# Performance work log

Measured on AMD Instinct MI355X. Metric: run time of the kernel, lower is better.

## Reference

```python
import jax, jax.numpy as jnp
import numpy as np

D = 2048      # in_features (model dim)
H = 1408      # d_intermediate (hidden per expert)
E = 16        # n_routed_experts
T = 16384     # flattened tokens
K = 4         # top_k experts per token


def setup_inputs() -> dict:
    key = jax.random.key(0)
    k1, k2, k3, k4, k5 = jax.random.split(key, 5)
    x = jax.random.normal(k1, (T, D), dtype=jnp.float32)
    weights = jax.random.uniform(k2, (T, K), dtype=jnp.float32)
    indices = jax.random.randint(k3, (T, K), 0, E)
    # Stacked GatedMLP params (bias=False as in mamba's GatedMLP):
    # fc1: [2H, D] per expert, fc2: [D, H] per expert
    W1 = jax.random.normal(k4, (E, 2 * H, D), dtype=jnp.float32) * (D ** -0.5)
    W2 = jax.random.normal(k5, (E, D, H), dtype=jnp.float32) * (H ** -0.5)
    return {"x": x, "weights": weights, "indices": indices, "W1": W1, "W2": W2}


def reference(x, weights, indices, W1, W2):
    # y[t] = sum_i ( GatedMLP_i(x[t]) * sum_k weights[t,k] * [indices[t,k]==i] )
    n_experts = W1.shape[0]
    y = jnp.zeros_like(x)
    for i in range(n_experts):  # small fixed expert loop
        # combined routing weight of expert i per token (handles duplicate hits like += in torch)
        cw = jnp.sum(weights * (indices == i), axis=-1)      # [T]
        h = x @ W1[i].T                                      # [T, 2H]
        u, g = jnp.split(h, 2, axis=-1)                      # chunk(2, dim=-1): (y, gate)
        out = (u * jax.nn.silu(g)) @ W2[i].T                 # [T, D]
        y = y + out * cw[:, None]
    return y
```

## Files before the change

kernel.cpp:

```cpp
#include <hip/hip_runtime.h>

#define D_ 2048
#define H_ 1408
#define E_ 16
#define T_ 16384
#define K_ 4
#define TK_ 65536
#define BM_ 256
#define BK_ 64
#define MAXT_ 272

typedef __attribute__((ext_vector_type(8))) short bf16x8;
typedef __attribute__((ext_vector_type(4))) float f32x4;
typedef __attribute__((ext_vector_type(4))) unsigned short u16x4;
typedef __attribute__((ext_vector_type(8))) unsigned short u16x8;

#define M_COUNTS 0
#define M_OFF    16
#define M_CUR    33
#define M_NT     49
#define M_TE     64
#define M_TR     (64 + MAXT_)
#define M_TN     (64 + 2*MAXT_)

#define XB_OFF   0ULL
#define W1B_OFF  67108864ULL
#define W2B_OFF  (W1B_OFF + 188743680ULL)
#define ACT_OFF  (W2B_OFF + 94371840ULL)
#define PERM_OFF (ACT_OFF + 184549376ULL)
#define WGT_OFF  (PERM_OFF + 262144ULL)
#define META_B   (WGT_OFF + 262144ULL)
#define INV_OFF  (META_B + 65536ULL)
#define YP_OFF   (INV_OFF + 262144ULL)
#define WS_NEED  (YP_OFF + 268435456ULL)

#define SBAR()  __builtin_amdgcn_s_barrier()
#define SCHED() __builtin_amdgcn_sched_barrier(0)
#define LGK0()  asm volatile("s_waitcnt lgkmcnt(0)" ::: "memory")
#define VM6()   asm volatile("s_waitcnt vmcnt(6)" ::: "memory")
#define PRIO1() __builtin_amdgcn_s_setprio(1)
#define PRIO0() __builtin_amdgcn_s_setprio(0)

static __device__ __forceinline__ unsigned short f2bf(float f) {
  unsigned u = __builtin_bit_cast(unsigned, f);
  u += 0x7fffu + ((u >> 16) & 1u);
  return (unsigned short)(u >> 16);
}
static __device__ __forceinline__ float bf2f(unsigned short s) {
  return __builtin_bit_cast(float, (unsigned)s << 16);
}

static __device__ __forceinline__ void gload16(const void* g, unsigned ldsOff) {
  __builtin_amdgcn_global_load_lds(
      (const __attribute__((address_space(1))) unsigned int*)(unsigned long long)g,
      (__attribute__((address_space(3))) unsigned int*)(unsigned long long)ldsOff,
      16, 0, 0);
}

__global__ void cvt_kernel(const float* __restrict__ in,
                           unsigned short* __restrict__ out, long long n) {
  long long i = ((long long)blockIdx.x * blockDim.x + threadIdx.x) * 4;
  const long long stride = (long long)gridDim.x * blockDim.x * 4;
  for (; i < n; i += stride) {
    float4 v = *reinterpret_cast<const float4*>(in + i);
    u16x4 o = { f2bf(v.x), f2bf(v.y), f2bf(v.z), f2bf(v.w) };
    *reinterpret_cast<u16x4*>(out + i) = o;
  }
}

__global__ void route_count(const int* __restrict__ idx, int* __restrict__ meta) {
  int i = blockIdx.x * 256 + threadIdx.x;
  if (i < TK_) atomicAdd(&meta[M_COUNTS + idx[i]], 1);
}

__global__ void scan_build(int* __restrict__ meta) {
  if (threadIdx.x != 0 || blockIdx.x != 0) return;
  int off = 0;
  for (int e = 0; e < E_; ++e) {
    meta[M_OFF + e] = off;
    meta[M_CUR + e] = off;
    off += meta[M_COUNTS + e];
  }
  meta[M_OFF + E_] = off;
  int nt = 0;
  for (int e = 0; e < E_; ++e) {
    int c = meta[M_COUNTS + e], b = meta[M_OFF + e];
    for (int r = 0; r < c; r += BM_) {
      meta[M_TE + nt] = e;
      meta[M_TR + nt] = b + r;
      meta[M_TN + nt] = (c - r < BM_) ? (c - r) : BM_;
      ++nt;
    }
  }
  meta[M_NT] = nt;
}

__global__ void route_fill(const int* __restrict__ idx, const float* __restrict__ wts,
                           int* __restrict__ meta, int* __restrict__ perm,
                           float* __restrict__ wgt, int* __restrict__ inv) {
  int i = blockIdx.x * 256 + threadIdx.x;
  if (i >= TK_) return;
  int e = idx[i];
  int pos = atomicAdd(&meta[M_CUR + e], 1);
  perm[pos] = i >> 2;
  wgt[pos] = wts[i];
  inv[i] = pos;
}

__global__ __launch_bounds__(512, 2) void gemm1_kernel(
    const char* __restrict__ xb, const char* __restrict__ w1b,
    const int* __restrict__ perm, const int* __restrict__ meta,
    unsigned short* __restrict__ act) {
  __shared__ char lds[131072];
  int bid = (int)blockIdx.x;
  bid = (bid & 7) * (int)(gridDim.x >> 3) + (bid >> 3);
  const int tb = bid / 11;
  const int cb = bid - tb * 11;
  if (tb >= meta[M_NT]) return;
  const int e = meta[M_TE + tb];
  const int row0 = meta[M_TR + tb];
  const int nrows = meta[M_TN + tb];
  const int tid = threadIdx.x, lane = tid & 63, wid = tid >> 6;
  const int wr = wid >> 2, wc = wid & 3;
  const unsigned ldsBase = (unsigned)(unsigned long long)&lds[0];
  constexpr int NT = D_ / BK_;

  const char* aSrc[4];
  const char* bSrc[4];
  {
    const int r8 = tid >> 3;
    const unsigned colb0 = (unsigned)(tid & 7) * 16u;
#pragma unroll
    for (int i = 0; i < 4; ++i) {
      const int r = r8 + i * 64;
      const unsigned colb = colb0 ^ ((unsigned)(r & 7) << 4);
      const int rc = (r < nrows) ? r : 0;
      aSrc[i] = xb + (size_t)perm[row0 + rc] * 4096 + colb;
      const int w1row = (i < 2) ? (cb * 128 + r) : (H_ + cb * 128 + (r - 128));
      bSrc[i] = w1b + (size_t)e * (2 * H_) * 4096ULL + (size_t)w1row * 4096 + colb;
    }
  }

  const int l15 = lane & 15, hi = lane >> 4;
  const unsigned swz = (unsigned)(l15 & 7) << 4;
  unsigned aOff[8], bOffU[2], bOffG[2];
#pragma unroll
  for (int m = 0; m < 8; ++m) {
    const int row = wr * 128 + m * 16 + l15;
    aOff[m] = (unsigned)(row * 128) + (((unsigned)hi * 16u) ^ swz);
  }
#pragma unroll
  for (int n = 0; n < 2; ++n) {
    const int ru = wc * 32 + n * 16 + l15;
    bOffU[n] = 65536u + (unsigned)(ru * 128) + (((unsigned)hi * 16u) ^ swz);
    const int rg = ru + 128;
    bOffG[n] = 65536u + (unsigned)(rg * 128) + (((unsigned)hi * 16u) ^ swz);
  }

  f32x4 aU[8][2], aG[8][2];
#pragma unroll
  for (int m = 0; m < 8; ++m)
#pragma unroll
    for (int n = 0; n < 2; ++n) {
      aU[m][n] = (f32x4){0.f, 0.f, 0.f, 0.f};
      aG[m][n] = (f32x4){0.f, 0.f, 0.f, 0.f};
    }

  auto STAGE_A = [&](int t, int h) {
    const int tt = (t < NT) ? t : (NT - 1);
    const size_t kb = (size_t)tt * 128;
    const unsigned dst = ldsBase + (unsigned)(t & 1) * 32768u + (unsigned)h * 16384u + (unsigned)tid * 16u;
    gload16(aSrc[h * 2 + 0] + kb, dst);
    gload16(aSrc[h * 2 + 1] + kb, dst + 8192u);
  };
  auto STAGE_B = [&](int t, int h) {
    const int tt = (t < NT) ? t : (NT - 1);
    const size_t kb = (size_t)tt * 128;
    const unsigned dst = ldsBase + 65536u + (unsigned)(t & 1) * 32768u + (unsigned)h * 16384u + (unsigned)tid * 16u;
    gload16(bSrc[h * 2 + 0] + kb, dst);
    gload16(bSrc[h * 2 + 1] + kb, dst + 8192u);
  };

  STAGE_B(0, 0); STAGE_B(0, 1); STAGE_A(0, 0); STAGE_A(0, 1);
  STAGE_B(1, 0); STAGE_B(1, 1); STAGE_A(1, 0);
  VM6(); SCHED(); SBAR();

  for (int t = 0; t < NT; ++t) {
    const char* base = lds + (unsigned)(t & 1) * 32768u;
    bf16x8 aLo[4][2], aHi[4][2], bu[2][2], bg[2][2];

#pragma unroll
    for (int m = 0; m < 4; ++m)
#pragma unroll
      for (int ks = 0; ks < 2; ++ks)
        aLo[m][ks] = *reinterpret_cast<const bf16x8*>(base + (aOff[m] ^ (unsigned)(ks << 6)));
#pragma unroll
    for (int n = 0; n < 2; ++n)
#pragma unroll
      for (int ks = 0; ks < 2; ++ks)
        bu[n][ks] = *reinterpret_cast<const bf16x8*>(base + (bOffU[n] ^ (unsigned)(ks << 6)));
    STAGE_A(t + 1, 1);
    SCHED(); SBAR(); LGK0(); SCHED();
    PRIO1();
#pragma unroll
    for (int ks = 0; ks < 2; ++ks)
#pragma unroll
      for (int m = 0; m < 4; ++m)
#pragma unroll
        for (int n = 0; n < 2; ++n)
          aU[m][n] = __builtin_amdgcn_mfma_f32_16x16x32_bf16(aLo[m][ks], bu[n][ks], aU[m][n], 0, 0, 0);
    PRIO0(); SCHED(); SBAR();

#pragma unroll
    for (int n = 0; n < 2; ++n)
#pragma unroll
      for (int ks = 0; ks < 2; ++ks)
        bg[n][ks] = *reinterpret_cast<const bf16x8*>(base + (bOffG[n] ^ (unsigned)(ks << 6)));
    STAGE_B(t + 2, 0);
    SCHED(); SBAR(); LGK0(); SCHED();
    PRIO1();
#pragma unroll
    for (int ks = 0; ks < 2; ++ks)
#pragma unroll
      for (int m = 0; m < 4; ++m)
#pragma unroll
        for (int n = 0; n < 2; ++n)
          aG[m][n] = __builtin_amdgcn_mfma_f32_16x16x32_bf16(aLo[m][ks], bg[n][ks], aG[m][n], 0, 0, 0);
    PRIO0(); SCHED(); SBAR();

#pragma unroll
    for (int m = 0; m < 4; ++m)
#pragma unroll
      for (int ks = 0; ks < 2; ++ks)
        aHi[m][ks] = *reinterpret_cast<const bf16x8*>(base + (aOff[4 + m] ^ (unsigned)(ks << 6)));
    STAGE_B(t + 2, 1);
    SCHED(); SBAR(); LGK0(); SCHED();
    PRIO1();
#pragma unroll
    for (int ks = 0; ks < 2; ++ks)
#pragma unroll
      for (int m = 0; m < 4; ++m)
#pragma unroll
        for (int n = 0; n < 2; ++n)
          aU[4 + m][n] = __builtin_amdgcn_mfma_f32_16x16x32_bf16(aHi[m][ks], bu[n][ks], aU[4 + m][n], 0, 0, 0);
    PRIO0(); SCHED(); SBAR();

    STAGE_A(t + 2, 0);
    VM6(); SCHED(); SBAR();
    PRIO1();
#pragma unroll
    for (int ks = 0; ks < 2; ++ks)
#pragma unroll
      for (int m = 0; m < 4; ++m)
#pragma unroll
        for (int n = 0; n < 2; ++n)
          aG[4 + m][n] = __builtin_amdgcn_mfma_f32_16x16x32_bf16(aHi[m][ks], bg[n][ks], aG[4 + m][n], 0, 0, 0);
    PRIO0(); SCHED(); SBAR();
  }

#pragma unroll
  for (int m = 0; m < 8; ++m)
#pragma unroll
    for (int j = 0; j < 4; ++j) {
      const int r = wr * 128 + m * 16 + hi * 4 + j;
      if (r < nrows) {
        const size_t rowBase = (size_t)(row0 + r) * H_ + (size_t)cb * 128 + (size_t)wc * 32;
#pragma unroll
        for (int n = 0; n < 2; ++n) {
          const float u = aU[m][n][j];
          const float g = aG[m][n][j];
          act[rowBase + n * 16 + l15] = f2bf(u * (g / (1.0f + __expf(-g))));
        }
      }
    }
}

template <int ATOMIC>
__global__ __launch_bounds__(512, 2) void gemm2_kernel(
    const char* __restrict__ actb, const char* __restrict__ w2b,
    const int* __restrict__ perm, const float* __restrict__ wgt,
    const int* __restrict__ meta, unsigned short* __restrict__ yp,
    float* __restrict__ y) {
  __shared__ char lds[131072];
  int bid = (int)blockIdx.x;
  bid = (bid & 7) * (int)(gridDim.x >> 3) + (bid >> 3);
  const int tb = bid >> 3;
  const int cb = bid & 7;
  if (tb >= meta[M_NT]) return;
  const int e = meta[M_TE + tb];
  const int row0 = meta[M_TR + tb];
  const int nrows = meta[M_TN + tb];
  const int tid = threadIdx.x, lane = tid & 63, wid = tid >> 6;
  const int wr = wid >> 2, wc = wid & 3;
  const unsigned ldsBase = (unsigned)(unsigned long long)&lds[0];
  constexpr int NT = H_ / BK_;

  const char* aSrc[4];
  const char* bSrc[4];
  {
    const int r8 = tid >> 3;
    const unsigned colb0 = (unsigned)(tid & 7) * 16u;
#pragma unroll
    for (int i = 0; i < 4; ++i) {
      const int r = r8 + i * 64;
      const unsigned colb = colb0 ^ ((unsigned)(r & 7) << 4);
      const int rc = (r < nrows) ? r : 0;
      aSrc[i] = actb + (size_t)(row0 + rc) * (H_ * 2) + colb;
      const int brow = cb * 256 + r;
      bSrc[i] = w2b + (size_t)e * D_ * (H_ * 2) + (size_t)brow * (H_ * 2) + colb;
    }
  }

  const int l15 = lane & 15, hi = lane >> 4;
  const unsigned swz = (unsigned)(l15 & 7) << 4;
  unsigned aOff[8], bOff[4];
#pragma unroll
  for (int m = 0; m < 8; ++m) {
    const int row = wr * 128 + m * 16 + l15;
    aOff[m] = (unsigned)(row * 128) + (((unsigned)hi * 16u) ^ swz);
  }
#pragma unroll
  for (int n = 0; n < 4; ++n) {
    const int rb = wc * 64 + n * 16 + l15;
    bOff[n] = 65536u + (unsigned)(rb * 128) + (((unsigned)hi * 16u) ^ swz);
  }

  f32x4 acc[8][4];
#pragma unroll
  for (int m = 0; m < 8; ++m)
#pragma unroll
    for (int n = 0; n < 4; ++n) acc[m][n] = (f32x4){0.f, 0.f, 0.f, 0.f};

  auto STAGE_A = [&](int t, int h) {
    const int tt = (t < NT) ? t : (NT - 1);
    const size_t kb = (size_t)tt * 128;
    const unsigned dst = ldsBase + (unsigned)(t & 1) * 32768u + (unsigned)h * 16384u + (unsigned)tid * 16u;
    gload16(aSrc[h * 2 + 0] + kb, dst);
    gload16(aSrc[h * 2 + 1] + kb, dst + 8192u);
  };
  auto STAGE_B = [&](int t, int h) {
    const int tt = (t < NT) ? t : (NT - 1);
    const size_t kb = (size_t)tt * 128;
    const unsigned dst = ldsBase + 65536u + (unsigned)(t & 1) * 32768u + (unsigned)h * 16384u + (unsigned)tid * 16u;
    gload16(bSrc[h * 2 + 0] + kb, dst);
    gload16(bSrc[h * 2 + 1] + kb, dst + 8192u);
  };

  STAGE_B(0, 0); STAGE_B(0, 1); STAGE_A(0, 0); STAGE_A(0, 1);
  STAGE_B(1, 0); STAGE_B(1, 1); STAGE_A(1, 0);
  VM6(); SCHED(); SBAR();

  for (int t = 0; t < NT; ++t) {
    const char* base = lds + (unsigned)(t & 1) * 32768u;
    bf16x8 aLo[4][2], aHi[4][2], b[4][2];

#pragma unroll
    for (int m = 0; m < 4; ++m)
#pragma unroll
      for (int ks = 0; ks < 2; ++ks)
        aLo[m][ks] = *reinterpret_cast<const bf16x8*>(base + (aOff[m] ^ (unsigned)(ks << 6)));
#pragma unroll
    for (int n = 0; n < 4; ++n)
#pragma unroll
      for (int ks = 0; ks < 2; ++ks)
        b[n][ks] = *reinterpret_cast<const bf16x8*>(base + (bOff[n] ^ (unsigned)(ks << 6)));
    STAGE_A(t + 1, 1);
    SCHED(); SBAR(); LGK0(); SCHED();
    PRIO1();
#pragma unroll
    for (int ks = 0; ks < 2; ++ks)
#pragma unroll
      for (int m = 0; m < 4; ++m)
#pragma unroll
        for (int n = 0; n < 2; ++n)
          acc[m][n] = __builtin_amdgcn_mfma_f32_16x16x32_bf16(aLo[m][ks], b[n][ks], acc[m][n], 0, 0, 0);
    PRIO0(); SCHED(); SBAR();

    STAGE_B(t + 2, 0);
    SCHED(); SBAR();
    PRIO1();
#pragma unroll
    for (int ks = 0; ks < 2; ++ks)
#pragma unroll
      for (int m = 0; m < 4; ++m)
#pragma unroll
        for (int n = 2; n < 4; ++n)
          acc[m][n] = __builtin_amdgcn_mfma_f32_16x16x32_bf16(aLo[m][ks], b[n][ks], acc[m][n], 0, 0, 0);
    PRIO0(); SCHED(); SBAR();

#pragma unroll
    for (int m = 0; m < 4; ++m)
#pragma unroll
      for (int ks = 0; ks < 2; ++ks)
        aHi[m][ks] = *reinterpret_cast<const bf16x8*>(base + (aOff[4 + m] ^ (unsigned)(ks << 6)));
    STAGE_B(t + 2, 1);
    SCHED(); SBAR(); LGK0(); SCHED();
    PRIO1();
#pragma unroll
    for (int ks = 0; ks < 2; ++ks)
#pragma unroll
      for (int m = 0; m < 4; ++m)
#pragma unroll
        for (int n = 0; n < 2; ++n)
          acc[4 + m][n] = __builtin_amdgcn_mfma_f32_16x16x32_bf16(aHi[m][ks], b[n][ks], acc[4 + m][n], 0, 0, 0);
    PRIO0(); SCHED(); SBAR();

    STAGE_A(t + 2, 0);
    VM6(); SCHED(); SBAR();
    PRIO1();
#pragma unroll
    for (int ks = 0; ks < 2; ++ks)
#pragma unroll
      for (int m = 0; m < 4; ++m)
#pragma unroll
        for (int n = 2; n < 4; ++n)
          acc[4 + m][n] = __builtin_amdgcn_mfma_f32_16x16x32_bf16(aHi[m][ks], b[n][ks], acc[4 + m][n], 0, 0, 0);
    PRIO0(); SCHED(); SBAR();
  }

#pragma unroll
  for (int m = 0; m < 8; ++m)
#pragma unroll
    for (int j = 0; j < 4; ++j) {
      const int r = wr * 128 + m * 16 + hi * 4 + j;
      if (r < nrows) {
        const float w = wgt[row0 + r];
        if (ATOMIC) {
          const int token = perm[row0 + r];
          float* yrow = y + (size_t)token * D_ + (size_t)cb * 256 + (size_t)wc * 64;
#pragma unroll
          for (int n = 0; n < 4; ++n)
            unsafeAtomicAdd(&yrow[n * 16 + l15], acc[m][n][j] * w);
        } else {
          unsigned short* prow = yp + (size_t)(row0 + r) * D_ + (size_t)cb * 256 + (size_t)wc * 64;
#pragma unroll
          for (int n = 0; n < 4; ++n)
            prow[n * 16 + l15] = f2bf(acc[m][n][j] * w);
        }
      }
    }
}

__global__ __launch_bounds__(256) void gather_kernel(
    const unsigned short* __restrict__ yp, const int* __restrict__ inv,
    float* __restrict__ y) {
  const int t = blockIdx.x;
  const int d0 = threadIdx.x * 8;
  int pos[4];
#pragma unroll
  for (int k = 0; k < 4; ++k) pos[k] = inv[t * 4 + k];
  float s[8];
#pragma unroll
  for (int i = 0; i < 8; ++i) s[i] = 0.f;
#pragma unroll
  for (int k = 0; k < 4; ++k) {
    u16x8 v = *reinterpret_cast<const u16x8*>(yp + (size_t)pos[k] * D_ + d0);
#pragma unroll
    for (int i = 0; i < 8; ++i) s[i] += bf2f(v[i]);
  }
  float4 lo = {s[0], s[1], s[2], s[3]}, hi4 = {s[4], s[5], s[6], s[7]};
  *reinterpret_cast<float4*>(y + (size_t)t * D_ + d0) = lo;
  *reinterpret_cast<float4*>(y + (size_t)t * D_ + d0 + 4) = hi4;
}

extern "C" void kernel_launch(void* const* d_in, const int* in_sizes, int n_in,
                              void* d_out, int out_size, void* d_ws, size_t ws_size,
                              hipStream_t stream) {
  const float* x   = (const float*)d_in[0];
  const float* wts = (const float*)d_in[1];
  const int*   idx = (const int*)d_in[2];
  const float* W1  = (const float*)d_in[3];
  const float* W2  = (const float*)d_in[4];
  float* y = (float*)d_out;
  char* ws = (char*)d_ws;

  unsigned short* xb  = (unsigned short*)(ws + XB_OFF);
  unsigned short* w1b = (unsigned short*)(ws + W1B_OFF);
  unsigned short* w2b = (unsigned short*)(ws + W2B_OFF);
  unsigned short* act = (unsigned short*)(ws + ACT_OFF);
  int*   perm = (int*)(ws + PERM_OFF);
  float* wgt  = (float*)(ws + WGT_OFF);
  int*   meta = (int*)(ws + META_B);
  int*   inv  = (int*)(ws + INV_OFF);
  unsigned short* yp = (unsigned short*)(ws + YP_OFF);

  const bool useYp = (ws_size >= (size_t)WS_NEED);

  hipMemsetAsync(meta, 0, 64 * sizeof(int), stream);
  if (!useYp) hipMemsetAsync(d_out, 0, (size_t)out_size * sizeof(float), stream);

  cvt_kernel<<<2048, 256, 0, stream>>>(x, xb, (long long)T_ * D_);
  cvt_kernel<<<2048, 256, 0, stream>>>(W1, w1b, (long long)E_ * 2 * H_ * D_);
  cvt_kernel<<<2048, 256, 0, stream>>>(W2, w2b, (long long)E_ * D_ * H_);

  route_count<<<TK_ / 256, 256, 0, stream>>>(idx, meta);
  scan_build<<<1, 64, 0, stream>>>(meta);
  route_fill<<<TK_ / 256, 256, 0, stream>>>(idx, wts, meta, perm, wgt, inv);

  gemm1_kernel<<<MAXT_ * (H_ / 128), 512, 0, stream>>>(
      (const char*)xb, (const char*)w1b, perm, meta, act);

  if (useYp) {
    gemm2_kernel<0><<<MAXT_ * (D_ / 256), 512, 0, stream>>>(
        (const char*)act, (const char*)w2b, perm, wgt, meta, yp, y);
    gather_kernel<<<T_, 256, 0, stream>>>(yp, inv, y);
  } else {
    gemm2_kernel<1><<<MAXT_ * (D_ / 256), 512, 0, stream>>>(
        (const char*)act, (const char*)w2b, perm, wgt, meta, yp, y);
  }
}
```

Baseline: 1.724 ms.

## Fuse fp32-to-bf16 weight conversion into GEMM B-tile loading

Drops the separate cvt passes over W1 and W2. Each GEMM now loads fp32 weight tiles into registers, packs them to bf16 with v_cvt_pk_bf16_f32, and writes them swizzled into LDS, with the wait counts in the pipeline adjusted to match. This removes a full read and write of the weights in bf16 form, but weight tiles are now read in fp32 by every token tile that uses them, which doubles B-side global traffic and adds register and conversion pressure inside the main loop.

```diff
diff --git a/kernel.cpp b/kernel.cpp
--- a/kernel.cpp
+++ b/kernel.cpp
@@ -14,6 +14,7 @@
 typedef __attribute__((ext_vector_type(4))) float f32x4;
 typedef __attribute__((ext_vector_type(4))) unsigned short u16x4;
 typedef __attribute__((ext_vector_type(8))) unsigned short u16x8;
+typedef __attribute__((ext_vector_type(4))) unsigned int u32x4;
 
 #define M_COUNTS 0
 #define M_OFF    16
@@ -24,9 +25,7 @@
 #define M_TN     (64 + 2*MAXT_)
 
 #define XB_OFF   0ULL
-#define W1B_OFF  67108864ULL
-#define W2B_OFF  (W1B_OFF + 188743680ULL)
-#define ACT_OFF  (W2B_OFF + 94371840ULL)
+#define ACT_OFF  67108864ULL
 #define PERM_OFF (ACT_OFF + 184549376ULL)
 #define WGT_OFF  (PERM_OFF + 262144ULL)
 #define META_B   (WGT_OFF + 262144ULL)
@@ -37,7 +36,7 @@
 #define SBAR()  __builtin_amdgcn_s_barrier()
 #define SCHED() __builtin_amdgcn_sched_barrier(0)
 #define LGK0()  asm volatile("s_waitcnt lgkmcnt(0)" ::: "memory")
-#define VM6()   asm volatile("s_waitcnt vmcnt(6)" ::: "memory")
+#define VM10()  asm volatile("s_waitcnt vmcnt(10)" ::: "memory")
 #define PRIO1() __builtin_amdgcn_s_setprio(1)
 #define PRIO0() __builtin_amdgcn_s_setprio(0)
 
@@ -48,6 +47,11 @@
 }
 static __device__ __forceinline__ float bf2f(unsigned short s) {
   return __builtin_bit_cast(float, (unsigned)s << 16);
+}
+static __device__ __forceinline__ unsigned pk2(float lo, float hi) {
+  unsigned r;
+  asm("v_cvt_pk_bf16_f32 %0, %1, %2" : "=v"(r) : "v"(lo), "v"(hi));
+  return r;
 }
 
 static __device__ __forceinline__ void gload16(const void* g, unsigned ldsOff) {
@@ -108,7 +112,7 @@
 }
 
 __global__ __launch_bounds__(512, 2) void gemm1_kernel(
-    const char* __restrict__ xb, const char* __restrict__ w1b,
+    const char* __restrict__ xb, const float* __restrict__ W1,
     const int* __restrict__ perm, const int* __restrict__ meta,
     unsigned short* __restrict__ act) {
   __shared__ char lds[131072];
@@ -126,7 +130,6 @@
   constexpr int NT = D_ / BK_;
 
   const char* aSrc[4];
-  const char* bSrc[4];
   {
     const int r8 = tid >> 3;
     const unsigned colb0 = (unsigned)(tid & 7) * 16u;
@@ -136,9 +139,13 @@
       const unsigned colb = colb0 ^ ((unsigned)(r & 7) << 4);
       const int rc = (r < nrows) ? r : 0;
       aSrc[i] = xb + (size_t)perm[row0 + rc] * 4096 + colb;
-      const int w1row = (i < 2) ? (cb * 128 + r) : (H_ + cb * 128 + (r - 128));
-      bSrc[i] = w1b + (size_t)e * (2 * H_) * 4096ULL + (size_t)w1row * 4096 + colb;
-    }
+    }
+  }
+  const float* bSrcF;
+  {
+    const int r = tid >> 1;
+    const int w1row = (r < 128) ? (cb * 128 + r) : (H_ + cb * 128 + (r - 128));
+    bSrcF = W1 + (size_t)e * (2 * H_) * D_ + (size_t)w1row * D_ + (tid & 1) * 32;
   }
 
   const int l15 = lane & 15, hi = lane >> 4;
@@ -173,17 +180,35 @@
     gload16(aSrc[h * 2 + 0] + kb, dst);
     gload16(aSrc[h * 2 + 1] + kb, dst + 8192u);
   };
-  auto STAGE_B = [&](int t, int h) {
+
+  float4 breg[8];
+  auto B_LOAD = [&](int t) {
     const int tt = (t < NT) ? t : (NT - 1);
-    const size_t kb = (size_t)tt * 128;
-    const unsigned dst = ldsBase + 65536u + (unsigned)(t & 1) * 32768u + (unsigned)h * 16384u + (unsigned)tid * 16u;
-    gload16(bSrc[h * 2 + 0] + kb, dst);
-    gload16(bSrc[h * 2 + 1] + kb, dst + 8192u);
+    const float* p = bSrcF + (size_t)tt * 64;
+#pragma unroll
+    for (int i = 0; i < 8; ++i) breg[i] = *reinterpret_cast<const float4*>(p + i * 4);
   };
-
-  STAGE_B(0, 0); STAGE_B(0, 1); STAGE_A(0, 0); STAGE_A(0, 1);
-  STAGE_B(1, 0); STAGE_B(1, 1); STAGE_A(1, 0);
-  VM6(); SCHED(); SBAR();
+  auto B_WRITE = [&](int t) {
+    char* wb = lds + 65536u + (unsigned)(t & 1) * 32768u + (unsigned)(tid >> 1) * 128u;
+    const unsigned wc0 = (unsigned)(tid & 1) * 64u;
+    const unsigned wsz = ((unsigned)((tid >> 1) & 7)) << 4;
+#pragma unroll
+    for (int j = 0; j < 4; ++j) {
+      u32x4 w;
+      w[0] = pk2(breg[2 * j + 0].x, breg[2 * j + 0].y);
+      w[1] = pk2(breg[2 * j + 0].z, breg[2 * j + 0].w);
+      w[2] = pk2(breg[2 * j + 1].x, breg[2 * j + 1].y);
+      w[3] = pk2(breg[2 * j + 1].z, breg[2 * j + 1].w);
+      *reinterpret_cast<u32x4*>(wb + ((wc0 + (unsigned)j * 16u) ^ wsz)) = w;
+    }
+  };
+
+  B_LOAD(0);
+  STAGE_A(0, 0); STAGE_A(0, 1);
+  B_WRITE(0);
+  B_LOAD(1);
+  STAGE_A(1, 0);
+  VM10(); LGK0(); SCHED(); SBAR();
 
   for (int t = 0; t < NT; ++t) {
     const char* base = lds + (unsigned)(t & 1) * 32768u;
@@ -216,7 +241,7 @@
 #pragma unroll
       for (int ks = 0; ks < 2; ++ks)
         bg[n][ks] = *reinterpret_cast<const bf16x8*>(base + (bOffG[n] ^ (unsigned)(ks << 6)));
-    STAGE_B(t + 2, 0);
+    B_WRITE(t + 1);
     SCHED(); SBAR(); LGK0(); SCHED();
     PRIO1();
 #pragma unroll
@@ -233,7 +258,7 @@
 #pragma unroll
       for (int ks = 0; ks < 2; ++ks)
         aHi[m][ks] = *reinterpret_cast<const bf16x8*>(base + (aOff[4 + m] ^ (unsigned)(ks << 6)));
-    STAGE_B(t + 2, 1);
+    B_LOAD(t + 2);
     SCHED(); SBAR(); LGK0(); SCHED();
     PRIO1();
 #pragma unroll
@@ -246,7 +271,7 @@
     PRIO0(); SCHED(); SBAR();
 
     STAGE_A(t + 2, 0);
-    VM6(); SCHED(); SBAR();
+    VM10(); SCHED(); SBAR();
     PRIO1();
 #pragma unroll
     for (int ks = 0; ks < 2; ++ks)
@@ -277,7 +302,7 @@
 
 template <int ATOMIC>
 __global__ __launch_bounds__(512, 2) void gemm2_kernel(
-    const char* __restrict__ actb, const char* __restrict__ w2b,
+    const char* __restrict__ actb, const float* __restrict__ W2,
     const int* __restrict__ perm, const float* __restrict__ wgt,
     const int* __restrict__ meta, unsigned short* __restrict__ yp,
     float* __restrict__ y) {
@@ -296,7 +321,6 @@
   constexpr int NT = H_ / BK_;
 
   const char* aSrc[4];
-  const char* bSrc[4];
   {
     const int r8 = tid >> 3;
     const unsigned colb0 = (unsigned)(tid & 7) * 16u;
@@ -306,9 +330,13 @@
       const unsigned colb = colb0 ^ ((unsigned)(r & 7) << 4);
       const int rc = (r < nrows) ? r : 0;
       aSrc[i] = actb + (size_t)(row0 + rc) * (H_ * 2) + colb;
-      const int brow = cb * 256 + r;
-      bSrc[i] = w2b + (size_t)e * D_ * (H_ * 2) + (size_t)brow * (H_ * 2) + colb;
-    }
+    }
+  }
+  const float* bSrcF;
+  {
+    const int r = tid >> 1;
+    const int w2row = cb * 256 + r;
+    bSrcF = W2 + (size_t)e * D_ * H_ + (size_t)w2row * H_ + (tid & 1) * 32;
   }
 
   const int l15 = lane & 15, hi = lane >> 4;
@@ -338,17 +366,35 @@
     gload16(aSrc[h * 2 + 0] + kb, dst);
     gload16(aSrc[h * 2 + 1] + kb, dst + 8192u);
   };
-  auto STAGE_B = [&](int t, int h) {
+
+  float4 breg[8];
+  auto B_LOAD = [&](int t) {
     const int tt = (t < NT) ? t : (NT - 1);
-    const size_t kb = (size_t)tt * 128;
-    const unsigned dst = ldsBase + 65536u + (unsigned)(t & 1) * 32768u + (unsigned)h * 16384u + (unsigned)tid * 16u;
-    gload16(bSrc[h * 2 + 0] + kb, dst);
-    gload16(bSrc[h * 2 + 1] + kb, dst + 8192u);
+    const float* p = bSrcF + (size_t)tt * 64;
+#pragma unroll
+    for (int i = 0; i < 8; ++i) breg[i] = *reinterpret_cast<const float4*>(p + i * 4);
   };
-
-  STAGE_B(0, 0); STAGE_B(0, 1); STAGE_A(0, 0); STAGE_A(0, 1);
-  STAGE_B(1, 0); STAGE_B(1, 1); STAGE_A(1, 0);
-  VM6(); SCHED(); SBAR();
+  auto B_WRITE = [&](int t) {
+    char* wb = lds + 65536u + (unsigned)(t & 1) * 32768u + (unsigned)(tid >> 1) * 128u;
+    const unsigned wc0 = (unsigned)(tid & 1) * 64u;
+    const unsigned wsz = ((unsigned)((tid >> 1) & 7)) << 4;
+#pragma unroll
+    for (int j = 0; j < 4; ++j) {
+      u32x4 w;
+      w[0] = pk2(breg[2 * j + 0].x, breg[2 * j + 0].y);
+      w[1] = pk2(breg[2 * j + 0].z, breg[2 * j + 0].w);
+      w[2] = pk2(breg[2 * j + 1].x, breg[2 * j + 1].y);
+      w[3] = pk2(breg[2 * j + 1].z, breg[2 * j + 1].w);
+      *reinterpret_cast<u32x4*>(wb + ((wc0 + (unsigned)j * 16u) ^ wsz)) = w;
+    }
+  };
+
+  B_LOAD(0);
+  STAGE_A(0, 0); STAGE_A(0, 1);
+  B_WRITE(0);
+  B_LOAD(1);
+  STAGE_A(1, 0);
+  VM10(); LGK0(); SCHED(); SBAR();
 
   for (int t = 0; t < NT; ++t) {
     const char* base = lds + (unsigned)(t & 1) * 32768u;
@@ -376,8 +422,8 @@
           acc[m][n] = __builtin_amdgcn_mfma_f32_16x16x32_bf16(aLo[m][ks], b[n][ks], acc[m][n], 0, 0, 0);
     PRIO0(); SCHED(); SBAR();
 
-    STAGE_B(t + 2, 0);
-    SCHED(); SBAR();
+    B_WRITE(t + 1);
+    SCHED(); SBAR(); LGK0(); SCHED();
     PRIO1();
 #pragma unroll
     for (int ks = 0; ks < 2; ++ks)
@@ -393,7 +439,7 @@
 #pragma unroll
       for (int ks = 0; ks < 2; ++ks)
         aHi[m][ks] = *reinterpret_cast<const bf16x8*>(base + (aOff[4 + m] ^ (unsigned)(ks << 6)));
-    STAGE_B(t + 2, 1);
+    B_LOAD(t + 2);
     SCHED(); SBAR(); LGK0(); SCHED();
     PRIO1();
 #pragma unroll
@@ -406,7 +452,7 @@
     PRIO0(); SCHED(); SBAR();
 
     STAGE_A(t + 2, 0);
-    VM6(); SCHED(); SBAR();
+    VM10(); SCHED(); SBAR();
     PRIO1();
 #pragma unroll
     for (int ks = 0; ks < 2; ++ks)
@@ -475,8 +521,6 @@
   char* ws = (char*)d_ws;
 
   unsigned short* xb  = (unsigned short*)(ws + XB_OFF);
-  unsigned short* w1b = (unsigned short*)(ws + W1B_OFF);
-  unsigned short* w2b = (unsigned short*)(ws + W2B_OFF);
   unsigned short* act = (unsigned short*)(ws + ACT_OFF);
   int*   perm = (int*)(ws + PERM_OFF);
   float* wgt  = (float*)(ws + WGT_OFF);
@@ -490,22 +534,20 @@
   if (!useYp) hipMemsetAsync(d_out, 0, (size_t)out_size * sizeof(float), stream);
 
   cvt_kernel<<<2048, 256, 0, stream>>>(x, xb, (long long)T_ * D_);
-  cvt_kernel<<<2048, 256, 0, stream>>>(W1, w1b, (long long)E_ * 2 * H_ * D_);
-  cvt_kernel<<<2048, 256, 0, stream>>>(W2, w2b, (long long)E_ * D_ * H_);
 
   route_count<<<TK_ / 256, 256, 0, stream>>>(idx, meta);
   scan_build<<<1, 64, 0, stream>>>(meta);
   route_fill<<<TK_ / 256, 256, 0, stream>>>(idx, wts, meta, perm, wgt, inv);
 
   gemm1_kernel<<<MAXT_ * (H_ / 128), 512, 0, stream>>>(
-      (const char*)xb, (const char*)w1b, perm, meta, act);
+      (const char*)xb, W1, perm, meta, act);
 
   if (useYp) {
     gemm2_kernel<0><<<MAXT_ * (D_ / 256), 512, 0, stream>>>(
-        (const char*)act, (const char*)w2b, perm, wgt, meta, yp, y);
+        (const char*)act, W2, perm, wgt, meta, yp, y);
     gather_kernel<<<T_, 256, 0, stream>>>(yp, inv, y);
   } else {
     gemm2_kernel<1><<<MAXT_ * (D_ / 256), 512, 0, stream>>>(
-        (const char*)act, (const char*)w2b, perm, wgt, meta, yp, y);
-  }
-}
+        (const char*)act, W2, perm, wgt, meta, yp, y);
+  }
+}
```

New measurement: 2.732 ms. 58.5% more time.
